# Kernel tuning notes

Measured on AMD Instinct MI355X. Metric: run time of the kernel, lower is better.

Reference implementation:

```python
import jax, jax.numpy as jnp
import numpy as np

NUM_TAGS = 24
B, S = 1024, 1024


def setup_inputs() -> dict:
    key = jax.random.key(0)
    k1, k2, k3, k4, k5 = jax.random.split(key, 5)
    feature = jax.random.normal(k1, (B, S, NUM_TAGS), dtype=jnp.float32)
    mask = jnp.ones((B, S), dtype=jnp.int32)
    target = jax.random.randint(k2, (B, S), 0, NUM_TAGS, dtype=jnp.int64)
    # CRF learned parameters (torchcrf inits uniform(-0.1, 0.1))
    start_transitions = jax.random.uniform(k3, (NUM_TAGS,), minval=-0.1, maxval=0.1, dtype=jnp.float32)
    end_transitions = jax.random.uniform(k4, (NUM_TAGS,), minval=-0.1, maxval=0.1, dtype=jnp.float32)
    transitions = jax.random.uniform(k5, (NUM_TAGS, NUM_TAGS), minval=-0.1, maxval=0.1, dtype=jnp.float32)
    return {"feature": feature, "mask": mask, "target": target,
            "start_transitions": start_transitions,
            "end_transitions": end_transitions,
            "transitions": transitions}


def _crf_neg_mean_llh(feature, mask, target, start_transitions, end_transitions, transitions):
    # torchcrf: batch_first -> transpose to time-major [S, B, ...]
    em = jnp.swapaxes(feature, 0, 1)           # [S, B, T]
    tags = jnp.swapaxes(target, 0, 1)          # [S, B]
    m = jnp.swapaxes(mask, 0, 1).astype(bool)  # [S, B]
    b_idx = jnp.arange(em.shape[1])

    # ---- numerator: score of the gold path (fully vectorized over time) ----
    score0 = start_transitions[tags[0]] + em[0, b_idx, tags[0]]          # [B]
    prev_t, cur_t = tags[:-1], tags[1:]                                   # [S-1, B]
    step_scores = transitions[prev_t, cur_t] + jnp.take_along_axis(
        em[1:], cur_t[:, :, None], axis=2)[:, :, 0]                       # [S-1, B]
    numerator = score0 + jnp.sum(step_scores * m[1:], axis=0)
    seq_ends = jnp.sum(m.astype(jnp.int32), axis=0) - 1                   # [B]
    last_tags = tags[seq_ends, b_idx]
    numerator = numerator + end_transitions[last_tags]

    # ---- denominator: forward algorithm (log-sum-exp DP over time) ----
    def step(score, inp):
        em_t, m_t = inp  # [B, T], [B]
        # score[b, i] + transitions[i, j] + em_t[b, j] -> lse over i
        nxt = jax.nn.logsumexp(score[:, :, None] + transitions[None, :, :]
                               + em_t[:, None, :], axis=1)
        score = jnp.where(m_t[:, None], nxt, score)
        return score, None

    init = start_transitions[None, :] + em[0]                             # [B, T]
    final, _ = jax.lax.scan(step, init, (em[1:], m[1:]))
    denominator = jax.nn.logsumexp(final + end_transitions[None, :], axis=1)

    llh = numerator - denominator      # [B]
    # reduction='mean' then .neg() in CRFCell
    return -jnp.mean(llh)


def reference(feature, mask, target, start_transitions, end_transitions, transitions):
    return _crf_neg_mean_llh(feature, mask, target,
                             start_transitions, end_transitions, transitions)
```

## Files before the change

### kernel.cpp

```cpp
#include <hip/hip_runtime.h>

#define NT 24
#define SQ 1024
#define NB 1024
#define NSEG 32
#define LSEG 32
#define TS 8
#define LPAD 194

typedef float f32x16 __attribute__((ext_vector_type(16)));
typedef short bf16x8 __attribute__((ext_vector_type(8)));
typedef unsigned int uint2v __attribute__((ext_vector_type(2)));

__device__ __forceinline__ unsigned short bfrnd(float x) {
    unsigned u = __float_as_uint(x);
    return (unsigned short)((u + 0x7fffu + ((u >> 16) & 1u)) >> 16);
}
__device__ __forceinline__ unsigned cvtpk(float lo, float hi) {
    unsigned r;
    asm("v_cvt_pk_bf16_f32 %0, %1, %2" : "=v"(r) : "v"(lo), "v"(hi));
    return r;
}

__device__ __forceinline__ void stage_issue(
    float4 (&pre)[24], unsigned long long& tg,
    const float* __restrict__ fbase, const unsigned long long* __restrict__ tagT,
    int t0, int sg, int sf, int b)
{
#pragma unroll
    for (int q = 0; q < 24; ++q) {
        int sb = 8 * (q & 3) + sg;
        int f4 = 8 * (q >> 2) + sf;
        pre[q] = *(const float4*)(fbase + ((size_t)sb * SQ + (size_t)t0) * NT + f4 * 4);
    }
    tg = tagT[(size_t)(t0 >> 3) * NB + b];
}

__device__ __forceinline__ void stage_write(
    const float4 (&pre)[24], float* __restrict__ ldsEm, int sg, int sf)
{
#pragma unroll
    for (int q = 0; q < 24; ++q) {
        int sb = 8 * (q & 3) + sg;
        int f4 = 8 * (q >> 2) + sf;
        float2* d = (float2*)&ldsEm[sb * LPAD + f4 * 4];
        d[0] = make_float2(pre[q].x, pre[q].y);
        d[1] = make_float2(pre[q].z, pre[q].w);
    }
}

template<int MODE>
__device__ __forceinline__ void tile_compute(
    unsigned long long tg64, unsigned pbyte,
    bf16x8 A1, bf16x8 A2,
    const float* __restrict__ ldsEm, const float* __restrict__ ldsT,
    const float* __restrict__ ldsS,
    int hi, int c, float (&w)[12], float& lz2, float& numAcc, int& cnt)
{
    if (MODE != 3) {
#pragma unroll
        for (int i = 0; i < 4; ++i) {
            int k = hi * 4 + i;
            int by = (int)(tg64 >> (8 * k)) & 255;
            int tg = by & 31;
            int m = by >> 7;
            int pv = (k == 0) ? (int)(pbyte & 31) : ((int)(tg64 >> (8 * k - 8)) & 31);
            float emv = ldsEm[c * LPAD + k * NT + tg];
            float contrib;
            if (MODE == 1 && hi == 0 && i == 0)
                contrib = ldsS[tg] + emv;
            else
                contrib = m ? (ldsT[pv * NT + tg] + emv) : 0.0f;
            numAcc += contrib;
            cnt += m;
        }
    }
#pragma unroll
    for (int k = 0; k < TS; ++k) {
        const float2* ep = (const float2*)&ldsEm[c * LPAD + k * NT + 4 * hi];
        float2 e0 = ep[0], e1 = ep[1], e2 = ep[4], e3 = ep[5], e4 = ep[8], e5 = ep[9];
        float ee[12] = {e0.x, e0.y, e1.x, e1.y, e2.x, e2.y,
                        e3.x, e3.y, e4.x, e4.y, e5.x, e5.y};
        if (MODE == 1 && k == 0) {
#pragma unroll
            for (int r = 0; r < 12; ++r) {
                int R = (r & 3) + 8 * (r >> 2) + 4 * hi;
                w[r] = __expf(ldsS[R] + ee[r]);
            }
            continue;
        }
        int m = (int)(tg64 >> (8 * k + 7)) & 1;
        unsigned aw = cvtpk(w[0], w[1]);
        unsigned bw = cvtpk(w[2], w[3]);
        unsigned cw = cvtpk(w[4], w[5]);
        unsigned dw = cvtpk(w[6], w[7]);
        unsigned ew = cvtpk(w[8], w[9]);
        unsigned fw = cvtpk(w[10], w[11]);
        uint2v s1 = __builtin_amdgcn_permlane32_swap(aw, cw, false, false);
        uint2v s2 = __builtin_amdgcn_permlane32_swap(bw, dw, false, false);
        uint2v s3 = __builtin_amdgcn_permlane32_swap(ew, 0u, false, false);
        uint2v s4 = __builtin_amdgcn_permlane32_swap(fw, 0u, false, false);
        union { unsigned u[4]; bf16x8 v; } B1, B2;
        B1.u[0] = s1[0]; B1.u[1] = s2[0]; B1.u[2] = s1[1]; B1.u[3] = s2[1];
        B2.u[0] = s3[0]; B2.u[1] = s4[0]; B2.u[2] = s3[1]; B2.u[3] = s4[1];
        f32x16 acc = {};
        acc = __builtin_amdgcn_mfma_f32_32x32x16_bf16(A1, B1.v, acc, 0, 0, 0);
        acc = __builtin_amdgcn_mfma_f32_32x32x16_bf16(A2, B2.v, acc, 0, 0, 0);
#pragma unroll
        for (int r = 0; r < 12; ++r) {
            float q = acc[r] * __expf(ee[r]);
            w[r] = m ? q : w[r];
        }
        if ((k & 3) == 3) {
            float zh = ((w[0] + w[1]) + (w[2] + w[3])) +
                       ((w[4] + w[5]) + (w[6] + w[7])) +
                       ((w[8] + w[9]) + (w[10] + w[11]));
            float zt = zh + __shfl_xor(zh, 32);
            float rz = __builtin_amdgcn_rcpf(zt);
            lz2 += __log2f(zt);
#pragma unroll
            for (int r = 0; r < 12; ++r) w[r] *= rz;
        }
    }
}

extern "C" __global__ void __launch_bounds__(128)
crf_pack(const int* __restrict__ target, const int* __restrict__ maskp,
         unsigned long long* __restrict__ tagT)
{
    const int b = blockIdx.x;
    const int oct = threadIdx.x;
    const int* tb = target + (size_t)b * SQ + oct * 8;
    const int* mb = maskp + (size_t)b * SQ + oct * 8;
    int4 t0 = *(const int4*)tb, t1 = *(const int4*)(tb + 4);
    int4 m0 = *(const int4*)mb, m1 = *(const int4*)(mb + 4);
    int tg[8] = {t0.x, t0.y, t0.z, t0.w, t1.x, t1.y, t1.z, t1.w};
    int mk[8] = {m0.x, m0.y, m0.z, m0.w, m1.x, m1.y, m1.z, m1.w};
    unsigned long long v = 0;
#pragma unroll
    for (int i = 0; i < 8; ++i)
        v |= (unsigned long long)((tg[i] & 31) | (mk[i] ? 128 : 0)) << (8 * i);
    tagT[(size_t)oct * NB + b] = v;
}

extern "C" __global__ void __launch_bounds__(64, 1)
crf_fwd(const float* __restrict__ feat,
        const float* __restrict__ startT, const float* __restrict__ endT,
        const float* __restrict__ trans,
        const unsigned long long* __restrict__ tagT,
        float* __restrict__ dP, float* __restrict__ nP, int* __restrict__ cP)
{
    __shared__ float ldsT[NT * NT];
    __shared__ float ldsS[NT];
    __shared__ float ldsE[NT];
    __shared__ __align__(16) float ldsEm[32 * LPAD];

    const int tid = threadIdx.x;
    const int hi = tid >> 5;
    const int c = tid & 31;
    const int sg = tid >> 3;
    const int sf = tid & 7;
    const int grp = blockIdx.x;
    const int bg = grp >> 5;
    const int p = grp & (NSEG - 1);
    const int b = bg * 32 + c;

    for (int i = tid; i < NT * NT; i += 64) ldsT[i] = trans[i];
    if (tid < NT) { ldsS[tid] = startT[tid]; ldsE[tid] = endT[tid]; }
    __syncthreads();

    union { unsigned short s[8]; bf16x8 v; } A1u, A2u;
#pragma unroll
    for (int j = 0; j < 8; ++j) {
        int k1 = 8 * hi + j;
        float v1 = (c < NT && k1 < NT) ? __expf(ldsT[k1 * NT + c]) : 0.0f;
        A1u.s[j] = bfrnd(v1);
        int k2 = 16 + 8 * hi + j;
        float v2 = (c < NT && k2 < NT) ? __expf(ldsT[k2 * NT + c]) : 0.0f;
        A2u.s[j] = bfrnd(v2);
    }

    const float* fbase = feat + (size_t)bg * 32 * SQ * NT;

    float w[12];
#pragma unroll
    for (int r = 0; r < 12; ++r) w[r] = 1.0f;
    float lz2 = 0.0f, sub2 = 0.0f, numAcc = 0.0f;
    int cnt = 0;
    unsigned pbyte = 0;
    const int a = p * LSEG;

    float4 pre[24];
    unsigned long long tgC, tgN;

    if (p > 0) {
        unsigned long long tgW;
        stage_issue(pre, tgW, fbase, tagT, a - TS, sg, sf, b);
        stage_write(pre, ldsEm, sg, sf);
        __syncthreads();
        stage_issue(pre, tgC, fbase, tagT, a, sg, sf, b);
        tile_compute<3>(tgW, pbyte, A1u.v, A2u.v, ldsEm, ldsT, ldsS,
                        hi, c, w, lz2, numAcc, cnt);
        pbyte = (unsigned)(tgW >> 56);
        float zh = ((w[0] + w[1]) + (w[2] + w[3])) + ((w[4] + w[5]) + (w[6] + w[7])) +
                   ((w[8] + w[9]) + (w[10] + w[11]));
        float zt = zh + __shfl_xor(zh, 32);
        sub2 = lz2 + __log2f(zt);
#pragma unroll 1
        for (int mt = 0; mt < 4; ++mt) {
            stage_write(pre, ldsEm, sg, sf);
            __syncthreads();
            tgN = 0;
            if (mt < 3) stage_issue(pre, tgN, fbase, tagT, a + TS * (mt + 1), sg, sf, b);
            tile_compute<0>(tgC, pbyte, A1u.v, A2u.v, ldsEm, ldsT, ldsS,
                            hi, c, w, lz2, numAcc, cnt);
            pbyte = (unsigned)(tgC >> 56);
            tgC = tgN;
        }
    } else {
        stage_issue(pre, tgC, fbase, tagT, 0, sg, sf, b);
        stage_write(pre, ldsEm, sg, sf);
        __syncthreads();
        stage_issue(pre, tgN, fbase, tagT, TS, sg, sf, b);
        tile_compute<1>(tgC, pbyte, A1u.v, A2u.v, ldsEm, ldsT, ldsS,
                        hi, c, w, lz2, numAcc, cnt);
        pbyte = (unsigned)(tgC >> 56);
        tgC = tgN;
#pragma unroll 1
        for (int mt = 1; mt < 4; ++mt) {
            stage_write(pre, ldsEm, sg, sf);
            __syncthreads();
            tgN = 0;
            if (mt < 3) stage_issue(pre, tgN, fbase, tagT, TS * (mt + 1), sg, sf, b);
            tile_compute<0>(tgC, pbyte, A1u.v, A2u.v, ldsEm, ldsT, ldsS,
                            hi, c, w, lz2, numAcc, cnt);
            pbyte = (unsigned)(tgC >> 56);
            tgC = tgN;
        }
    }

    float ze = 0.0f;
#pragma unroll
    for (int r = 0; r < 12; ++r) {
        int R = (r & 3) + 8 * (r >> 2) + 4 * hi;
        float wv = w[r];
        if (p == NSEG - 1) wv *= __expf(ldsE[R]);
        ze += wv;
    }
    float zt = ze + __shfl_xor(ze, 32);
    float res = (lz2 + __log2f(zt) - sub2) * 0.6931471805599453f;
    float ntot = numAcc + __shfl_xor(numAcc, 32);
    int ctot = cnt + __shfl_xor(cnt, 32);
    if (hi == 0) {
        dP[p * NB + b] = res;
        nP[p * NB + b] = ntot;
        cP[p * NB + b] = ctot;
    }
}

extern "C" __global__ void __launch_bounds__(64)
crf_combine(const float* __restrict__ dP, const float* __restrict__ nP,
            const int* __restrict__ cP, const int* __restrict__ target,
            const float* __restrict__ endT, float* __restrict__ bpart)
{
    const int b = blockIdx.x * 64 + threadIdx.x;
    float den = 0.f, num = 0.f;
    int cnt = 0;
#pragma unroll 8
    for (int p = 0; p < NSEG; ++p) {
        den += dP[p * NB + b];
        num += nP[p * NB + b];
        cnt += cP[p * NB + b];
    }
    int lastTag = target[(size_t)b * SQ + (cnt - 1)];
    float llh = (num + endT[lastTag]) - den;
#pragma unroll
    for (int m = 1; m < 64; m <<= 1) llh += __shfl_xor(llh, m, 64);
    if (threadIdx.x == 0) bpart[blockIdx.x] = llh;
}

extern "C" __global__ void __launch_bounds__(64)
crf_final(const float* __restrict__ bpart, float* __restrict__ out)
{
    float s = (threadIdx.x < NB / 64) ? bpart[threadIdx.x] : 0.0f;
#pragma unroll
    for (int m = 1; m < 64; m <<= 1) s += __shfl_xor(s, m, 64);
    if (threadIdx.x == 0) out[0] = -s * (1.0f / NB);
}

extern "C" void kernel_launch(void* const* d_in, const int* in_sizes, int n_in,
                              void* d_out, int out_size, void* d_ws, size_t ws_size,
                              hipStream_t stream)
{
    const float* feat   = (const float*)d_in[0];
    const int*   maskp  = (const int*)d_in[1];
    const int*   target = (const int*)d_in[2];
    const float* startT = (const float*)d_in[3];
    const float* endT   = (const float*)d_in[4];
    const float* trans  = (const float*)d_in[5];

    unsigned long long* tagT = (unsigned long long*)d_ws;
    float* dP = (float*)(tagT + (SQ / 8) * NB);
    float* nP = dP + NSEG * NB;
    int*   cP = (int*)(nP + NSEG * NB);
    float* bpart = (float*)(cP + NSEG * NB);

    crf_pack<<<NB, 128, 0, stream>>>(target, maskp, tagT);
    crf_fwd<<<(NB / 32) * NSEG, 64, 0, stream>>>(feat, startT, endT, trans, tagT,
                                                 dP, nP, cP);
    crf_combine<<<NB / 64, 64, 0, stream>>>(dP, nP, cP, target, endT, bpart);
    crf_final<<<1, 64, 0, stream>>>(bpart, (float*)d_out);
}
```

Before: 47.40 us.

## Split sequence into 64 short segments and stage emissions as bf16 in LDS

Halves the segment length (NSEG 32→64, LSEG 16), so twice as many blocks each run a shorter serial forward recurrence. The emission tile now goes into LDS as packed bf16 in a tag-group-major layout, which cuts LDS footprint and allows two blocks per CU via launch bounds. The per-segment loops are replaced by straight-line code. The trade-offs: the 8-step warm-up becomes a larger share of each segment, and the gold-path numerator now reads bf16-rounded emissions, losing some precision.

```diff
diff --git a/kernel.cpp b/kernel.cpp
--- a/kernel.cpp
+++ b/kernel.cpp
@@ -3,14 +3,14 @@
 #define NT 24
 #define SQ 1024
 #define NB 1024
-#define NSEG 32
-#define LSEG 32
+#define NSEG 64
+#define LSEG 16
 #define TS 8
-#define LPAD 194
 
 typedef float f32x16 __attribute__((ext_vector_type(16)));
 typedef short bf16x8 __attribute__((ext_vector_type(8)));
 typedef unsigned int uint2v __attribute__((ext_vector_type(2)));
+typedef unsigned long long u64;
 
 __device__ __forceinline__ unsigned short bfrnd(float x) {
     unsigned u = __float_as_uint(x);
@@ -21,42 +21,42 @@
     asm("v_cvt_pk_bf16_f32 %0, %1, %2" : "=v"(r) : "v"(lo), "v"(hi));
     return r;
 }
+__device__ __forceinline__ float bflo(unsigned p) { return __uint_as_float(p << 16); }
+__device__ __forceinline__ float bfhi(unsigned p) { return __uint_as_float(p & 0xffff0000u); }
 
 __device__ __forceinline__ void stage_issue(
-    float4 (&pre)[24], unsigned long long& tg,
-    const float* __restrict__ fbase, const unsigned long long* __restrict__ tagT,
-    int t0, int sg, int sf, int b)
+    float4 (&pre)[24], const float* __restrict__ fbase, int t0, int sg, int sf)
 {
 #pragma unroll
     for (int q = 0; q < 24; ++q) {
         int sb = 8 * (q & 3) + sg;
         int f4 = 8 * (q >> 2) + sf;
-        pre[q] = *(const float4*)(fbase + ((size_t)sb * SQ + (size_t)t0) * NT + f4 * 4);
-    }
-    tg = tagT[(size_t)(t0 >> 3) * NB + b];
+        pre[q] = *(const float4*)(fbase + (size_t)sb * SQ * NT + (size_t)t0 * NT + f4 * 4);
+    }
 }
 
 __device__ __forceinline__ void stage_write(
-    const float4 (&pre)[24], float* __restrict__ ldsEm, int sg, int sf)
+    const float4 (&pre)[24], u64* __restrict__ ldsX, int sg, int sf)
 {
 #pragma unroll
     for (int q = 0; q < 24; ++q) {
         int sb = 8 * (q & 3) + sg;
         int f4 = 8 * (q >> 2) + sf;
-        float2* d = (float2*)&ldsEm[sb * LPAD + f4 * 4];
-        d[0] = make_float2(pre[q].x, pre[q].y);
-        d[1] = make_float2(pre[q].z, pre[q].w);
+        int tl = f4 / 6, j4 = f4 % 6;
+        unsigned lo = cvtpk(pre[q].x, pre[q].y);
+        unsigned hi2 = cvtpk(pre[q].z, pre[q].w);
+        ldsX[(tl * 6 + j4) * 32 + sb] = ((u64)hi2 << 32) | lo;
     }
 }
 
 template<int MODE>
 __device__ __forceinline__ void tile_compute(
-    unsigned long long tg64, unsigned pbyte,
-    bf16x8 A1, bf16x8 A2,
-    const float* __restrict__ ldsEm, const float* __restrict__ ldsT,
+    u64 tg64, unsigned pbyte, bf16x8 A1, bf16x8 A2,
+    const u64* __restrict__ ldsX, const float* __restrict__ ldsT,
     const float* __restrict__ ldsS,
     int hi, int c, float (&w)[12], float& lz2, float& numAcc, int& cnt)
 {
+    const unsigned short* lds16 = (const unsigned short*)ldsX;
     if (MODE != 3) {
 #pragma unroll
         for (int i = 0; i < 4; ++i) {
@@ -65,7 +65,8 @@
             int tg = by & 31;
             int m = by >> 7;
             int pv = (k == 0) ? (int)(pbyte & 31) : ((int)(tg64 >> (8 * k - 8)) & 31);
-            float emv = ldsEm[c * LPAD + k * NT + tg];
+            float emv = __uint_as_float(
+                (unsigned)lds16[((k * 6 + (tg >> 2)) * 32 + c) * 4 + (tg & 3)] << 16);
             float contrib;
             if (MODE == 1 && hi == 0 && i == 0)
                 contrib = ldsS[tg] + emv;
@@ -77,10 +78,16 @@
     }
 #pragma unroll
     for (int k = 0; k < TS; ++k) {
-        const float2* ep = (const float2*)&ldsEm[c * LPAD + k * NT + 4 * hi];
-        float2 e0 = ep[0], e1 = ep[1], e2 = ep[4], e3 = ep[5], e4 = ep[8], e5 = ep[9];
-        float ee[12] = {e0.x, e0.y, e1.x, e1.y, e2.x, e2.y,
-                        e3.x, e3.y, e4.x, e4.y, e5.x, e5.y};
+        const u64* xk = ldsX + k * 6 * 32;
+        u64 d0 = xk[(hi + 0) * 32 + c];
+        u64 d1 = xk[(hi + 2) * 32 + c];
+        u64 d2 = xk[(hi + 4) * 32 + c];
+        unsigned l0 = (unsigned)d0, h0 = (unsigned)(d0 >> 32);
+        unsigned l1 = (unsigned)d1, h1 = (unsigned)(d1 >> 32);
+        unsigned l2 = (unsigned)d2, h2 = (unsigned)(d2 >> 32);
+        float ee[12] = {bflo(l0), bfhi(l0), bflo(h0), bfhi(h0),
+                        bflo(l1), bfhi(l1), bflo(h1), bfhi(h1),
+                        bflo(l2), bfhi(l2), bflo(h2), bfhi(h2)};
         if (MODE == 1 && k == 0) {
 #pragma unroll
             for (int r = 0; r < 12; ++r) {
@@ -126,7 +133,7 @@
 
 extern "C" __global__ void __launch_bounds__(128)
 crf_pack(const int* __restrict__ target, const int* __restrict__ maskp,
-         unsigned long long* __restrict__ tagT)
+         u64* __restrict__ tagT)
 {
     const int b = blockIdx.x;
     const int oct = threadIdx.x;
@@ -136,24 +143,24 @@
     int4 m0 = *(const int4*)mb, m1 = *(const int4*)(mb + 4);
     int tg[8] = {t0.x, t0.y, t0.z, t0.w, t1.x, t1.y, t1.z, t1.w};
     int mk[8] = {m0.x, m0.y, m0.z, m0.w, m1.x, m1.y, m1.z, m1.w};
-    unsigned long long v = 0;
+    u64 v = 0;
 #pragma unroll
     for (int i = 0; i < 8; ++i)
-        v |= (unsigned long long)((tg[i] & 31) | (mk[i] ? 128 : 0)) << (8 * i);
+        v |= (u64)((tg[i] & 31) | (mk[i] ? 128 : 0)) << (8 * i);
     tagT[(size_t)oct * NB + b] = v;
 }
 
-extern "C" __global__ void __launch_bounds__(64, 1)
+extern "C" __global__ void __launch_bounds__(64, 2)
 crf_fwd(const float* __restrict__ feat,
         const float* __restrict__ startT, const float* __restrict__ endT,
         const float* __restrict__ trans,
-        const unsigned long long* __restrict__ tagT,
+        const u64* __restrict__ tagT,
         float* __restrict__ dP, float* __restrict__ nP, int* __restrict__ cP)
 {
     __shared__ float ldsT[NT * NT];
     __shared__ float ldsS[NT];
     __shared__ float ldsE[NT];
-    __shared__ __align__(16) float ldsEm[32 * LPAD];
+    __shared__ __align__(16) u64 ldsX[TS * 6 * 32];
 
     const int tid = threadIdx.x;
     const int hi = tid >> 5;
@@ -161,7 +168,7 @@
     const int sg = tid >> 3;
     const int sf = tid & 7;
     const int grp = blockIdx.x;
-    const int bg = grp >> 5;
+    const int bg = grp >> 6;
     const int p = grp & (NSEG - 1);
     const int b = bg * 32 + c;
 
@@ -187,56 +194,44 @@
     for (int r = 0; r < 12; ++r) w[r] = 1.0f;
     float lz2 = 0.0f, sub2 = 0.0f, numAcc = 0.0f;
     int cnt = 0;
-    unsigned pbyte = 0;
     const int a = p * LSEG;
 
     float4 pre[24];
-    unsigned long long tgC, tgN;
+    u64 tg0 = tagT[(size_t)(a >> 3) * NB + b];
+    u64 tg1 = tagT[(size_t)((a + 8) >> 3) * NB + b];
 
     if (p > 0) {
-        unsigned long long tgW;
-        stage_issue(pre, tgW, fbase, tagT, a - TS, sg, sf, b);
-        stage_write(pre, ldsEm, sg, sf);
-        __syncthreads();
-        stage_issue(pre, tgC, fbase, tagT, a, sg, sf, b);
-        tile_compute<3>(tgW, pbyte, A1u.v, A2u.v, ldsEm, ldsT, ldsS,
-                        hi, c, w, lz2, numAcc, cnt);
-        pbyte = (unsigned)(tgW >> 56);
+        u64 tgW = tagT[(size_t)((a - 8) >> 3) * NB + b];
+        stage_issue(pre, fbase, a - 8, sg, sf);
+        stage_write(pre, ldsX, sg, sf);
+        __syncthreads();
+        stage_issue(pre, fbase, a, sg, sf);
+        tile_compute<3>(tgW, 0, A1u.v, A2u.v, ldsX, ldsT, ldsS,
+                        hi, c, w, lz2, numAcc, cnt);
         float zh = ((w[0] + w[1]) + (w[2] + w[3])) + ((w[4] + w[5]) + (w[6] + w[7])) +
                    ((w[8] + w[9]) + (w[10] + w[11]));
         float zt = zh + __shfl_xor(zh, 32);
         sub2 = lz2 + __log2f(zt);
-#pragma unroll 1
-        for (int mt = 0; mt < 4; ++mt) {
-            stage_write(pre, ldsEm, sg, sf);
-            __syncthreads();
-            tgN = 0;
-            if (mt < 3) stage_issue(pre, tgN, fbase, tagT, a + TS * (mt + 1), sg, sf, b);
-            tile_compute<0>(tgC, pbyte, A1u.v, A2u.v, ldsEm, ldsT, ldsS,
-                            hi, c, w, lz2, numAcc, cnt);
-            pbyte = (unsigned)(tgC >> 56);
-            tgC = tgN;
-        }
+        stage_write(pre, ldsX, sg, sf);
+        __syncthreads();
+        stage_issue(pre, fbase, a + 8, sg, sf);
+        tile_compute<0>(tg0, (unsigned)(tgW >> 56), A1u.v, A2u.v, ldsX, ldsT, ldsS,
+                        hi, c, w, lz2, numAcc, cnt);
+        stage_write(pre, ldsX, sg, sf);
+        __syncthreads();
+        tile_compute<0>(tg1, (unsigned)(tg0 >> 56), A1u.v, A2u.v, ldsX, ldsT, ldsS,
+                        hi, c, w, lz2, numAcc, cnt);
     } else {
-        stage_issue(pre, tgC, fbase, tagT, 0, sg, sf, b);
-        stage_write(pre, ldsEm, sg, sf);
-        __syncthreads();
-        stage_issue(pre, tgN, fbase, tagT, TS, sg, sf, b);
-        tile_compute<1>(tgC, pbyte, A1u.v, A2u.v, ldsEm, ldsT, ldsS,
-                        hi, c, w, lz2, numAcc, cnt);
-        pbyte = (unsigned)(tgC >> 56);
-        tgC = tgN;
-#pragma unroll 1
-        for (int mt = 1; mt < 4; ++mt) {
-            stage_write(pre, ldsEm, sg, sf);
-            __syncthreads();
-            tgN = 0;
-            if (mt < 3) stage_issue(pre, tgN, fbase, tagT, TS * (mt + 1), sg, sf, b);
-            tile_compute<0>(tgC, pbyte, A1u.v, A2u.v, ldsEm, ldsT, ldsS,
-                            hi, c, w, lz2, numAcc, cnt);
-            pbyte = (unsigned)(tgC >> 56);
-            tgC = tgN;
-        }
+        stage_issue(pre, fbase, 0, sg, sf);
+        stage_write(pre, ldsX, sg, sf);
+        __syncthreads();
+        stage_issue(pre, fbase, 8, sg, sf);
+        tile_compute<1>(tg0, 0, A1u.v, A2u.v, ldsX, ldsT, ldsS,
+                        hi, c, w, lz2, numAcc, cnt);
+        stage_write(pre, ldsX, sg, sf);
+        __syncthreads();
+        tile_compute<0>(tg1, (unsigned)(tg0 >> 56), A1u.v, A2u.v, ldsX, ldsT, ldsS,
+                        hi, c, w, lz2, numAcc, cnt);
     }
 
     float ze = 0.0f;
@@ -299,7 +294,7 @@
     const float* endT   = (const float*)d_in[4];
     const float* trans  = (const float*)d_in[5];
 
-    unsigned long long* tagT = (unsigned long long*)d_ws;
+    u64*   tagT = (u64*)d_ws;
     float* dP = (float*)(tagT + (SQ / 8) * NB);
     float* nP = dP + NSEG * NB;
     int*   cP = (int*)(nP + NSEG * NB);
```

Result: slower. 50.22 us (+5.9%).
